# Kernel optimization log

Hardware: AMD Instinct MI355X
Metric: run time of the kernel (lower is better)

Reference implementation:

```python
import jax, jax.numpy as jnp
import numpy as np

N, D, K = 131072, 64, 4096


def setup_inputs() -> dict:
    key = jax.random.key(0)
    k1, k2 = jax.random.split(key)
    x = jax.random.normal(k1, (N, D), dtype=jnp.float32)
    embed = jax.random.normal(k2, (K, D), dtype=jnp.float32)
    return {"x": x, "embed": embed}


def reference(x, embed):
    """EuclideanCodebook forward.

    x:     [N, D] flat input vectors
    embed: [K, D] codebook
    Returns (quantize [N,D], embed_ind [N], cluster_size [K], embed_sum [K,D]).
    cluster_size / embed_sum are the one-hot scatter statistics fed to the
    EMA codebook update (embed_onehot.sum(0) and flatten^T @ embed_onehot).
    """
    num_codes = embed.shape[0]
    x2 = jnp.sum(x * x, axis=-1, keepdims=True)               # [N, 1]
    e2 = jnp.sum(embed * embed, axis=-1)                      # [K]
    dist = x2 - 2.0 * (x @ embed.T) + e2[None, :]             # [N, K]
    embed_ind = jnp.argmin(dist, axis=-1)                     # [N]
    quantize = embed[embed_ind]                               # gather [N, D]
    # scatter statistics for EMA update
    cluster_size = jnp.zeros((num_codes,), x.dtype).at[embed_ind].add(1.0)  # [K]
    embed_sum = jax.ops.segment_sum(x, embed_ind, num_segments=num_codes)   # [K, D]
    return quantize, embed_ind, cluster_size, embed_sum
```

## Files before the change

kernel.cpp:

```cpp
#include <hip/hip_runtime.h>

#define N_ROWS 131072
#define DIM 64
#define K_CODES 4096
#define BROWS 256
#define CK 64
#define NCH (K_CODES / CK)
#define EST 72
#define EPS 0.015625f

typedef __attribute__((ext_vector_type(8))) short short8;
typedef __attribute__((ext_vector_type(4))) float f32x4;

__device__ inline unsigned short bf16rn(float f) {
    unsigned int u = __float_as_uint(f);
    u += 0x7FFFu + ((u >> 16) & 1u);
    return (unsigned short)(u >> 16);
}
__device__ inline unsigned int fkey(float f) {
    unsigned int u = __float_as_uint(f);
    return (u & 0x80000000u) ? ~u : (u | 0x80000000u);
}

__global__ void e2_kernel(const float* __restrict__ embed, float* __restrict__ e2) {
    int k = blockIdx.x * blockDim.x + threadIdx.x;
    const float4* e = reinterpret_cast<const float4*>(embed + (size_t)k * DIM);
    float s = 0.f;
#pragma unroll
    for (int i = 0; i < DIM / 4; ++i) {
        float4 v = e[i];
        s = fmaf(v.x, v.x, s);
        s = fmaf(v.y, v.y, s);
        s = fmaf(v.z, v.z, s);
        s = fmaf(v.w, v.w, s);
    }
    e2[k] = s;
}

__global__ __launch_bounds__(256, 2) void dist_argmin_kernel(
        const float* __restrict__ x, const float* __restrict__ embed,
        const float* __restrict__ e2g, int* __restrict__ ind_ws,
        float* __restrict__ ind_out, int* __restrict__ cnt,
        int* __restrict__ list) {
    __shared__ unsigned short esh[CK * EST];
    __shared__ unsigned short esl[CK * EST];
    __shared__ float e2s[CK];

    const int tid  = threadIdx.x;
    const int l15  = tid & 15;
    const int quad = (tid >> 4) & 3;
    const int wave = tid >> 6;
    const int r0w  = blockIdx.x * BROWS + wave * 64;

    short8 ah[4][2], al[4][2];
#pragma unroll
    for (int i = 0; i < 4; ++i)
#pragma unroll
        for (int s = 0; s < 2; ++s) {
            const float* xp = x + (size_t)(r0w + 16 * i + l15) * DIM + 32 * s + 8 * quad;
            float4 f0 = *(const float4*)xp;
            float4 f1 = *(const float4*)(xp + 4);
            float w[8] = {f0.x, f0.y, f0.z, f0.w, f1.x, f1.y, f1.z, f1.w};
            short8 h, l;
#pragma unroll
            for (int j = 0; j < 8; ++j) {
                unsigned short hb = bf16rn(w[j]);
                float hf = __uint_as_float(((unsigned int)hb) << 16);
                h[j] = (short)hb;
                l[j] = (short)bf16rn(w[j] - hf);
            }
            ah[i][s] = h;
            al[i][s] = l;
        }

    float s1[16], s2[16];
    int c1[16];
#pragma unroll
    for (int t = 0; t < 16; ++t) { s1[t] = 3.4e38f; s2[t] = 3.4e38f; c1[t] = 0; }

    for (int ch = 0; ch < NCH; ++ch) {
        const int c0 = ch * CK;
        __syncthreads();
        {
            const int col = tid >> 2;
            const int dq  = (tid & 3) * 16;
            const float* ep = embed + (size_t)(c0 + col) * DIM + dq;
            float4 a = *(const float4*)ep,       b = *(const float4*)(ep + 4),
                   c = *(const float4*)(ep + 8), d = *(const float4*)(ep + 12);
            float w[16] = {a.x, a.y, a.z, a.w, b.x, b.y, b.z, b.w,
                           c.x, c.y, c.z, c.w, d.x, d.y, d.z, d.w};
            unsigned short hb[16], lb[16];
#pragma unroll
            for (int j = 0; j < 16; ++j) {
                hb[j] = bf16rn(w[j]);
                float hf = __uint_as_float(((unsigned int)hb[j]) << 16);
                lb[j] = bf16rn(w[j] - hf);
            }
            *(uint4*)(&esh[col * EST + dq])     = *(uint4*)(hb);
            *(uint4*)(&esh[col * EST + dq + 8]) = *(uint4*)(hb + 8);
            *(uint4*)(&esl[col * EST + dq])     = *(uint4*)(lb);
            *(uint4*)(&esl[col * EST + dq + 8]) = *(uint4*)(lb + 8);
            if (tid < CK) e2s[tid] = e2g[c0 + tid];
        }
        __syncthreads();

        f32x4 acc[4][4];
#pragma unroll
        for (int i = 0; i < 4; ++i)
#pragma unroll
            for (int j = 0; j < 4; ++j) acc[i][j] = (f32x4){0.f, 0.f, 0.f, 0.f};

#pragma unroll
        for (int j = 0; j < 4; ++j) {
            const int cb = (16 * j + l15) * EST + 8 * quad;
            short8 bh0 = *(const short8*)(&esh[cb]);
            short8 bh1 = *(const short8*)(&esh[cb + 32]);
            short8 bl0 = *(const short8*)(&esl[cb]);
            short8 bl1 = *(const short8*)(&esl[cb + 32]);
#pragma unroll
            for (int i = 0; i < 4; ++i) {
                f32x4 a = acc[i][j];
                a = __builtin_amdgcn_mfma_f32_16x16x32_bf16(ah[i][0], bh0, a, 0, 0, 0);
                a = __builtin_amdgcn_mfma_f32_16x16x32_bf16(ah[i][1], bh1, a, 0, 0, 0);
                a = __builtin_amdgcn_mfma_f32_16x16x32_bf16(ah[i][0], bl0, a, 0, 0, 0);
                a = __builtin_amdgcn_mfma_f32_16x16x32_bf16(ah[i][1], bl1, a, 0, 0, 0);
                a = __builtin_amdgcn_mfma_f32_16x16x32_bf16(al[i][0], bh0, a, 0, 0, 0);
                a = __builtin_amdgcn_mfma_f32_16x16x32_bf16(al[i][1], bh1, a, 0, 0, 0);
                acc[i][j] = a;
            }
        }

#pragma unroll
        for (int j = 0; j < 4; ++j) {
            const int c = c0 + 16 * j + l15;
            const float e2v = e2s[16 * j + l15];
#pragma unroll
            for (int i = 0; i < 4; ++i)
#pragma unroll
                for (int r = 0; r < 4; ++r) {
                    float sc = fmaf(-2.f, acc[i][j][r], e2v);
                    const int st = i * 4 + r;
                    bool lt = sc < s1[st];
                    s2[st] = lt ? s1[st] : fminf(s2[st], sc);
                    c1[st] = lt ? c : c1[st];
                    s1[st] = lt ? sc : s1[st];
                }
        }
    }

#pragma unroll
    for (int st = 0; st < 16; ++st) {
#pragma unroll
        for (int m = 1; m < 16; m <<= 1) {
            float os1 = __shfl_xor(s1[st], m, 64);
            float os2 = __shfl_xor(s2[st], m, 64);
            int   oc1 = __shfl_xor(c1[st], m, 64);
            bool take = (os1 < s1[st]) || (os1 == s1[st] && oc1 < c1[st]);
            float loser = take ? s1[st] : os1;
            s2[st] = fminf(fminf(s2[st], os2), loser);
            if (take) { s1[st] = os1; c1[st] = oc1; }
        }
    }
    if (l15 == 0) {
#pragma unroll
        for (int st = 0; st < 16; ++st) {
            const int i = st >> 2, r = st & 3;
            const int row = r0w + 16 * i + 4 * quad + r;
            ind_ws[row] = c1[st];
            ind_out[row] = (float)c1[st];
            if (s2[st] - s1[st] < EPS) {
                int p = atomicAdd(cnt, 1);
                list[p] = row;
            }
        }
    }
}

__global__ void refine_kernel(const float* __restrict__ x,
                              const float* __restrict__ embed,
                              const float* __restrict__ e2g,
                              const int* __restrict__ cnt,
                              const int* __restrict__ list,
                              int* __restrict__ ind_ws,
                              float* __restrict__ ind_out) {
    __shared__ float xr[DIM];
    __shared__ unsigned long long red[256];
    const int tid = threadIdx.x;
    const int n = *cnt;
    for (int f = blockIdx.x; f < n; f += gridDim.x) {
        const int row = list[f];
        __syncthreads();
        if (tid < 16)
            ((float4*)xr)[tid] = ((const float4*)(x + (size_t)row * DIM))[tid];
        __syncthreads();
        unsigned long long best = ~0ull;
        for (int c = tid; c < K_CODES; c += 256) {
            const float4* ep = (const float4*)(embed + (size_t)c * DIM);
            float d0 = 0.f, d1 = 0.f, d2 = 0.f, d3 = 0.f;
#pragma unroll
            for (int q = 0; q < 16; ++q) {
                float4 ev = ep[q];
                d0 = fmaf(xr[4 * q + 0], ev.x, d0);
                d1 = fmaf(xr[4 * q + 1], ev.y, d1);
                d2 = fmaf(xr[4 * q + 2], ev.z, d2);
                d3 = fmaf(xr[4 * q + 3], ev.w, d3);
            }
            float sc = fmaf(-2.f, (d0 + d1) + (d2 + d3), e2g[c]);
            unsigned long long key =
                ((unsigned long long)fkey(sc) << 32) | (unsigned int)c;
            if (key < best) best = key;
        }
        red[tid] = best;
        __syncthreads();
        for (int w = 128; w > 0; w >>= 1) {
            if (tid < w && red[tid + w] < red[tid]) red[tid] = red[tid + w];
            __syncthreads();
        }
        if (tid == 0) {
            int k = (int)(red[0] & 0xFFFFFFFFull);
            ind_ws[row] = k;
            ind_out[row] = (float)k;
        }
    }
}

__global__ void scatter_kernel(const float* __restrict__ x,
                               const float* __restrict__ embed,
                               const int* __restrict__ ind,
                               float* __restrict__ quant,
                               float* __restrict__ cs,
                               float* __restrict__ esum) {
    const int t = blockIdx.x * blockDim.x + threadIdx.x;
    const int row = t >> 6;
    const int d = t & 63;
    const int k = ind[row];
    quant[t] = embed[(size_t)k * DIM + d];
    atomicAdd(&esum[(size_t)k * DIM + d], x[t]);
    if (d == 0) atomicAdd(&cs[k], 1.0f);
}

extern "C" void kernel_launch(void* const* d_in, const int* in_sizes, int n_in,
                              void* d_out, int out_size, void* d_ws, size_t ws_size,
                              hipStream_t stream) {
    const float* x     = (const float*)d_in[0];
    const float* embed = (const float*)d_in[1];

    float* out     = (float*)d_out;
    float* quant   = out;
    float* ind_out = out + (size_t)N_ROWS * DIM;
    float* cs      = ind_out + N_ROWS;
    float* esum    = cs + K_CODES;

    float* e2   = (float*)d_ws;
    int* cnt    = (int*)(e2 + K_CODES);
    int* list   = cnt + 4;
    int* ind_ws = list + N_ROWS;

    hipMemsetAsync(cs, 0, (size_t)(K_CODES + K_CODES * DIM) * sizeof(float), stream);
    hipMemsetAsync(cnt, 0, sizeof(int), stream);

    e2_kernel<<<K_CODES / 256, 256, 0, stream>>>(embed, e2);
    dist_argmin_kernel<<<N_ROWS / BROWS, 256, 0, stream>>>(
        x, embed, e2, ind_ws, ind_out, cnt, list);
    refine_kernel<<<256, 256, 0, stream>>>(x, embed, e2, cnt, list, ind_ws, ind_out);
    scatter_kernel<<<(size_t)N_ROWS * DIM / 256, 256, 0, stream>>>(
        x, embed, ind_ws, quant, cs, esum);
}
```

Measured before the change: 477.0 us.

## Precompute MFMA-layout bf16 codebook, fold e2 into accumulator, parallelize refine and scatter

A prep kernel now writes the codebook once as split hi/lo bf16 in the exact MFMA fragment order. The distance kernel reads those fragments straight from global memory, so it no longer converts in LDS per block or syncs per chunk. The -2 factor moves into x, the e2 term initialises the accumulator, and the tie threshold is tightened. Refinement changes to one row per lane, with the code range split across blockIdx.y and merged by 64-bit atomicMin plus an unpack kernel. The scatter uses float4 rows into four partitioned accumulators, followed by a reduce kernel to cut atomic contention. Risks are a smaller EPS that may miss near-ties, and more kernel launches.

```diff
diff --git a/kernel.cpp b/kernel.cpp
--- a/kernel.cpp
+++ b/kernel.cpp
@@ -3,11 +3,9 @@
 #define N_ROWS 131072
 #define DIM 64
 #define K_CODES 4096
-#define BROWS 256
-#define CK 64
-#define NCH (K_CODES / CK)
-#define EST 72
-#define EPS 0.015625f
+#define NCH (K_CODES / 64)
+#define P_PARTS 4
+#define EPS 0.00390625f
 
 typedef __attribute__((ext_vector_type(8))) short short8;
 typedef __attribute__((ext_vector_type(4))) float f32x4;
@@ -17,40 +15,59 @@
     u += 0x7FFFu + ((u >> 16) & 1u);
     return (unsigned short)(u >> 16);
 }
+__device__ inline float bfhi(unsigned short h) {
+    return __uint_as_float(((unsigned int)h) << 16);
+}
 __device__ inline unsigned int fkey(float f) {
     unsigned int u = __float_as_uint(f);
     return (u & 0x80000000u) ? ~u : (u | 0x80000000u);
 }
 
-__global__ void e2_kernel(const float* __restrict__ embed, float* __restrict__ e2) {
-    int k = blockIdx.x * blockDim.x + threadIdx.x;
-    const float4* e = reinterpret_cast<const float4*>(embed + (size_t)k * DIM);
+__global__ void prep_kernel(const float* __restrict__ embed,
+                            uint4* __restrict__ fh, uint4* __restrict__ fl,
+                            float* __restrict__ e2) {
+    const int c = blockIdx.x * blockDim.x + threadIdx.x;
+    float w[DIM];
+    const float4* ep = (const float4*)(embed + (size_t)c * DIM);
     float s = 0.f;
 #pragma unroll
-    for (int i = 0; i < DIM / 4; ++i) {
-        float4 v = e[i];
-        s = fmaf(v.x, v.x, s);
-        s = fmaf(v.y, v.y, s);
-        s = fmaf(v.z, v.z, s);
-        s = fmaf(v.w, v.w, s);
-    }
-    e2[k] = s;
+    for (int i = 0; i < 16; ++i) {
+        float4 v = ep[i];
+        w[4 * i] = v.x; w[4 * i + 1] = v.y; w[4 * i + 2] = v.z; w[4 * i + 3] = v.w;
+        s = fmaf(v.x, v.x, s); s = fmaf(v.y, v.y, s);
+        s = fmaf(v.z, v.z, s); s = fmaf(v.w, v.w, s);
+    }
+    e2[c] = s;
+    const size_t base = (size_t)(c >> 6) * 512 + ((c >> 4) & 3) * 128 + (c & 15);
+#pragma unroll
+    for (int sd = 0; sd < 2; ++sd)
+#pragma unroll
+        for (int q = 0; q < 4; ++q) {
+            unsigned short hb[8], lb[8];
+#pragma unroll
+            for (int m = 0; m < 8; ++m) {
+                float v = w[32 * sd + 8 * q + m];
+                hb[m] = bf16rn(v);
+                lb[m] = bf16rn(v - bfhi(hb[m]));
+            }
+            const size_t off = base + sd * 64 + q * 16;
+            fh[off] = *(uint4*)hb;
+            fl[off] = *(uint4*)lb;
+        }
 }
 
 __global__ __launch_bounds__(256, 2) void dist_argmin_kernel(
-        const float* __restrict__ x, const float* __restrict__ embed,
-        const float* __restrict__ e2g, int* __restrict__ ind_ws,
-        float* __restrict__ ind_out, int* __restrict__ cnt,
-        int* __restrict__ list) {
-    __shared__ unsigned short esh[CK * EST];
-    __shared__ unsigned short esl[CK * EST];
-    __shared__ float e2s[CK];
-
-    const int tid  = threadIdx.x;
-    const int l15  = tid & 15;
+        const float* __restrict__ x,
+        const short8* __restrict__ fh, const short8* __restrict__ fl,
+        const float* __restrict__ e2g,
+        int* __restrict__ ind_ws, float* __restrict__ ind_out,
+        int* __restrict__ cnt, int* __restrict__ list,
+        unsigned long long* __restrict__ pk) {
+    const int tid = threadIdx.x;
+    const int lane = tid & 63;
+    const int l15 = tid & 15;
     const int quad = (tid >> 4) & 3;
-    const int wave = tid >> 6;
-    const int r0w  = blockIdx.x * BROWS + wave * 64;
+    const int r0w = blockIdx.x * 256 + (tid >> 6) * 64;
 
     short8 ah[4][2], al[4][2];
 #pragma unroll
@@ -63,14 +80,13 @@
             float w[8] = {f0.x, f0.y, f0.z, f0.w, f1.x, f1.y, f1.z, f1.w};
             short8 h, l;
 #pragma unroll
-            for (int j = 0; j < 8; ++j) {
-                unsigned short hb = bf16rn(w[j]);
-                float hf = __uint_as_float(((unsigned int)hb) << 16);
-                h[j] = (short)hb;
-                l[j] = (short)bf16rn(w[j] - hf);
-            }
-            ah[i][s] = h;
-            al[i][s] = l;
+            for (int m = 0; m < 8; ++m) {
+                float v = -2.f * w[m];
+                unsigned short hb = bf16rn(v);
+                h[m] = (short)hb;
+                l[m] = (short)bf16rn(v - bfhi(hb));
+            }
+            ah[i][s] = h; al[i][s] = l;
         }
 
     float s1[16], s2[16];
@@ -78,74 +94,39 @@
 #pragma unroll
     for (int t = 0; t < 16; ++t) { s1[t] = 3.4e38f; s2[t] = 3.4e38f; c1[t] = 0; }
 
+    const short8* ph = fh + lane;
+    const short8* pl = fl + lane;
     for (int ch = 0; ch < NCH; ++ch) {
-        const int c0 = ch * CK;
-        __syncthreads();
-        {
-            const int col = tid >> 2;
-            const int dq  = (tid & 3) * 16;
-            const float* ep = embed + (size_t)(c0 + col) * DIM + dq;
-            float4 a = *(const float4*)ep,       b = *(const float4*)(ep + 4),
-                   c = *(const float4*)(ep + 8), d = *(const float4*)(ep + 12);
-            float w[16] = {a.x, a.y, a.z, a.w, b.x, b.y, b.z, b.w,
-                           c.x, c.y, c.z, c.w, d.x, d.y, d.z, d.w};
-            unsigned short hb[16], lb[16];
-#pragma unroll
-            for (int j = 0; j < 16; ++j) {
-                hb[j] = bf16rn(w[j]);
-                float hf = __uint_as_float(((unsigned int)hb[j]) << 16);
-                lb[j] = bf16rn(w[j] - hf);
-            }
-            *(uint4*)(&esh[col * EST + dq])     = *(uint4*)(hb);
-            *(uint4*)(&esh[col * EST + dq + 8]) = *(uint4*)(hb + 8);
-            *(uint4*)(&esl[col * EST + dq])     = *(uint4*)(lb);
-            *(uint4*)(&esl[col * EST + dq + 8]) = *(uint4*)(lb + 8);
-            if (tid < CK) e2s[tid] = e2g[c0 + tid];
-        }
-        __syncthreads();
-
-        f32x4 acc[4][4];
-#pragma unroll
-        for (int i = 0; i < 4; ++i)
-#pragma unroll
-            for (int j = 0; j < 4; ++j) acc[i][j] = (f32x4){0.f, 0.f, 0.f, 0.f};
-
 #pragma unroll
         for (int j = 0; j < 4; ++j) {
-            const int cb = (16 * j + l15) * EST + 8 * quad;
-            short8 bh0 = *(const short8*)(&esh[cb]);
-            short8 bh1 = *(const short8*)(&esh[cb + 32]);
-            short8 bl0 = *(const short8*)(&esl[cb]);
-            short8 bl1 = *(const short8*)(&esl[cb + 32]);
+            short8 bh0 = ph[(j * 2 + 0) * 64];
+            short8 bh1 = ph[(j * 2 + 1) * 64];
+            short8 bl0 = pl[(j * 2 + 0) * 64];
+            short8 bl1 = pl[(j * 2 + 1) * 64];
+            const float e2v = e2g[ch * 64 + 16 * j + l15];
+            const f32x4 cinit = {e2v, e2v, e2v, e2v};
+            const int cc = ch * 64 + 16 * j + l15;
 #pragma unroll
             for (int i = 0; i < 4; ++i) {
-                f32x4 a = acc[i][j];
-                a = __builtin_amdgcn_mfma_f32_16x16x32_bf16(ah[i][0], bh0, a, 0, 0, 0);
+                f32x4 a;
+                a = __builtin_amdgcn_mfma_f32_16x16x32_bf16(ah[i][0], bh0, cinit, 0, 0, 0);
                 a = __builtin_amdgcn_mfma_f32_16x16x32_bf16(ah[i][1], bh1, a, 0, 0, 0);
                 a = __builtin_amdgcn_mfma_f32_16x16x32_bf16(ah[i][0], bl0, a, 0, 0, 0);
                 a = __builtin_amdgcn_mfma_f32_16x16x32_bf16(ah[i][1], bl1, a, 0, 0, 0);
                 a = __builtin_amdgcn_mfma_f32_16x16x32_bf16(al[i][0], bh0, a, 0, 0, 0);
                 a = __builtin_amdgcn_mfma_f32_16x16x32_bf16(al[i][1], bh1, a, 0, 0, 0);
-                acc[i][j] = a;
-            }
-        }
-
-#pragma unroll
-        for (int j = 0; j < 4; ++j) {
-            const int c = c0 + 16 * j + l15;
-            const float e2v = e2s[16 * j + l15];
-#pragma unroll
-            for (int i = 0; i < 4; ++i)
 #pragma unroll
                 for (int r = 0; r < 4; ++r) {
-                    float sc = fmaf(-2.f, acc[i][j][r], e2v);
+                    const float sc = a[r];
                     const int st = i * 4 + r;
-                    bool lt = sc < s1[st];
-                    s2[st] = lt ? s1[st] : fminf(s2[st], sc);
-                    c1[st] = lt ? c : c1[st];
+                    const bool lt = sc < s1[st];
+                    s2[st] = fminf(fmaxf(sc, s1[st]), s2[st]);
+                    c1[st] = lt ? cc : c1[st];
                     s1[st] = lt ? sc : s1[st];
                 }
-        }
+            }
+        }
+        ph += 512; pl += 512;
     }
 
 #pragma unroll
@@ -164,13 +145,13 @@
     if (l15 == 0) {
 #pragma unroll
         for (int st = 0; st < 16; ++st) {
-            const int i = st >> 2, r = st & 3;
-            const int row = r0w + 16 * i + 4 * quad + r;
+            const int row = r0w + 16 * (st >> 2) + 4 * quad + (st & 3);
             ind_ws[row] = c1[st];
             ind_out[row] = (float)c1[st];
             if (s2[st] - s1[st] < EPS) {
                 int p = atomicAdd(cnt, 1);
                 list[p] = row;
+                pk[row] = ~0ull;
             }
         }
     }
@@ -181,26 +162,31 @@
                               const float* __restrict__ e2g,
                               const int* __restrict__ cnt,
                               const int* __restrict__ list,
-                              int* __restrict__ ind_ws,
-                              float* __restrict__ ind_out) {
-    __shared__ float xr[DIM];
-    __shared__ unsigned long long red[256];
-    const int tid = threadIdx.x;
+                              unsigned long long* __restrict__ pk) {
     const int n = *cnt;
-    for (int f = blockIdx.x; f < n; f += gridDim.x) {
-        const int row = list[f];
-        __syncthreads();
-        if (tid < 16)
-            ((float4*)xr)[tid] = ((const float4*)(x + (size_t)row * DIM))[tid];
-        __syncthreads();
+    if (n == 0) return;
+    const int lane = threadIdx.x & 63;
+    const int wv = threadIdx.x >> 6;
+    for (int base = blockIdx.x * 64; base < n; base += gridDim.x * 64) {
+        const int idx = base + lane;
+        const int srow = list[idx < n ? idx : n - 1];
+        float xr[DIM];
+        const float4* xp = (const float4*)(x + (size_t)srow * DIM);
+#pragma unroll
+        for (int q = 0; q < 16; ++q) {
+            float4 v = xp[q];
+            xr[4 * q] = v.x; xr[4 * q + 1] = v.y;
+            xr[4 * q + 2] = v.z; xr[4 * q + 3] = v.w;
+        }
+        const int c0 = blockIdx.y * 1024 + wv * 256;
         unsigned long long best = ~0ull;
-        for (int c = tid; c < K_CODES; c += 256) {
+        for (int c = c0; c < c0 + 256; ++c) {
             const float4* ep = (const float4*)(embed + (size_t)c * DIM);
             float d0 = 0.f, d1 = 0.f, d2 = 0.f, d3 = 0.f;
 #pragma unroll
             for (int q = 0; q < 16; ++q) {
                 float4 ev = ep[q];
-                d0 = fmaf(xr[4 * q + 0], ev.x, d0);
+                d0 = fmaf(xr[4 * q], ev.x, d0);
                 d1 = fmaf(xr[4 * q + 1], ev.y, d1);
                 d2 = fmaf(xr[4 * q + 2], ev.z, d2);
                 d3 = fmaf(xr[4 * q + 3], ev.w, d3);
@@ -210,33 +196,57 @@
                 ((unsigned long long)fkey(sc) << 32) | (unsigned int)c;
             if (key < best) best = key;
         }
-        red[tid] = best;
-        __syncthreads();
-        for (int w = 128; w > 0; w >>= 1) {
-            if (tid < w && red[tid + w] < red[tid]) red[tid] = red[tid + w];
-            __syncthreads();
-        }
-        if (tid == 0) {
-            int k = (int)(red[0] & 0xFFFFFFFFull);
-            ind_ws[row] = k;
-            ind_out[row] = (float)k;
-        }
-    }
+        atomicMin(&pk[srow], best);
+    }
+}
+
+__global__ void unpack_kernel(const int* __restrict__ cnt,
+                              const int* __restrict__ list,
+                              const unsigned long long* __restrict__ pk,
+                              int* __restrict__ ind_ws,
+                              float* __restrict__ ind_out) {
+    const int i = blockIdx.x * blockDim.x + threadIdx.x;
+    if (i >= *cnt) return;
+    const int row = list[i];
+    const int k = (int)(pk[row] & 0xFFFFFFFFull);
+    ind_ws[row] = k;
+    ind_out[row] = (float)k;
 }
 
 __global__ void scatter_kernel(const float* __restrict__ x,
                                const float* __restrict__ embed,
                                const int* __restrict__ ind,
                                float* __restrict__ quant,
-                               float* __restrict__ cs,
-                               float* __restrict__ esum) {
+                               float* __restrict__ cs_p,
+                               float* __restrict__ esum_p) {
     const int t = blockIdx.x * blockDim.x + threadIdx.x;
-    const int row = t >> 6;
-    const int d = t & 63;
+    const int row = t >> 4;
+    const int dq = (t & 15) * 4;
     const int k = ind[row];
-    quant[t] = embed[(size_t)k * DIM + d];
-    atomicAdd(&esum[(size_t)k * DIM + d], x[t]);
-    if (d == 0) atomicAdd(&cs[k], 1.0f);
+    const int part = blockIdx.x & (P_PARTS - 1);
+    float4 xv = *(const float4*)(x + (size_t)row * DIM + dq);
+    *(float4*)(quant + (size_t)row * DIM + dq) =
+        *(const float4*)(embed + (size_t)k * DIM + dq);
+    float* ep = esum_p + ((size_t)part * K_CODES + k) * DIM + dq;
+    atomicAdd(ep + 0, xv.x); atomicAdd(ep + 1, xv.y);
+    atomicAdd(ep + 2, xv.z); atomicAdd(ep + 3, xv.w);
+    if ((t & 15) == 0) atomicAdd(cs_p + part * K_CODES + k, 1.0f);
+}
+
+__global__ void reduce_kernel(const float* __restrict__ esum_p,
+                              const float* __restrict__ cs_p,
+                              float* __restrict__ esum, float* __restrict__ cs) {
+    const int i = blockIdx.x * blockDim.x + threadIdx.x;
+    float s = 0.f;
+#pragma unroll
+    for (int p = 0; p < P_PARTS; ++p) s += esum_p[(size_t)p * K_CODES * DIM + i];
+    esum[i] = s;
+    if (i < K_CODES) {
+        float c = 0.f;
+#pragma unroll
+        for (int p = 0; p < P_PARTS; ++p) c += cs_p[p * K_CODES + i];
+        cs[i] = c;
+    }
 }
 
 extern "C" void kernel_launch(void* const* d_in, const int* in_sizes, int n_in,
@@ -251,18 +261,27 @@
     float* cs      = ind_out + N_ROWS;
     float* esum    = cs + K_CODES;
 
-    float* e2   = (float*)d_ws;
-    int* cnt    = (int*)(e2 + K_CODES);
-    int* list   = cnt + 4;
-    int* ind_ws = list + N_ROWS;
-
-    hipMemsetAsync(cs, 0, (size_t)(K_CODES + K_CODES * DIM) * sizeof(float), stream);
-    hipMemsetAsync(cnt, 0, sizeof(int), stream);
-
-    e2_kernel<<<K_CODES / 256, 256, 0, stream>>>(embed, e2);
-    dist_argmin_kernel<<<N_ROWS / BROWS, 256, 0, stream>>>(
-        x, embed, e2, ind_ws, ind_out, cnt, list);
-    refine_kernel<<<256, 256, 0, stream>>>(x, embed, e2, cnt, list, ind_ws, ind_out);
-    scatter_kernel<<<(size_t)N_ROWS * DIM / 256, 256, 0, stream>>>(
-        x, embed, ind_ws, quant, cs, esum);
-}
+    char* w = (char*)d_ws;
+    unsigned long long* pk = (unsigned long long*)w;          w += (size_t)N_ROWS * 8;
+    short8* fh   = (short8*)w;                                w += (size_t)K_CODES * DIM * 2;
+    short8* fl   = (short8*)w;                                w += (size_t)K_CODES * DIM * 2;
+    float*  e2   = (float*)w;                                 w += K_CODES * 4;
+    int*    list = (int*)w;                                   w += (size_t)N_ROWS * 4;
+    int*    ind_ws = (int*)w;                                 w += (size_t)N_ROWS * 4;
+    int*    cnt  = (int*)w;                                   w += 16;
+    float*  esum_p = (float*)w;                               w += (size_t)P_PARTS * K_CODES * DIM * 4;
+    float*  cs_p = (float*)w;
+
+    hipMemsetAsync(cnt, 0, 4, stream);
+    hipMemsetAsync(esum_p, 0,
+                   (size_t)P_PARTS * (K_CODES * DIM + K_CODES) * 4, stream);
+
+    prep_kernel<<<K_CODES / 256, 256, 0, stream>>>(embed, (uint4*)fh, (uint4*)fl, e2);
+    dist_argmin_kernel<<<N_ROWS / 256, 256, 0, stream>>>(
+        x, fh, fl, e2, ind_ws, ind_out, cnt, list, pk);
+    refine_kernel<<<dim3(64, 4), 256, 0, stream>>>(x, embed, e2, cnt, list, pk);
+    unpack_kernel<<<N_ROWS / 256, 256, 0, stream>>>(cnt, list, pk, ind_ws, ind_out);
+    scatter_kernel<<<(size_t)N_ROWS * 16 / 256, 256, 0, stream>>>(
+        x, embed, ind_ws, quant, cs_p, esum_p);
+    reduce_kernel<<<K_CODES * DIM / 256, 256, 0, stream>>>(esum_p, cs_p, esum, cs);
+}
```

After: 733.5 us. +53.8%, slower.
